# Kernel optimization log

Measured on AMD Instinct MI355X. Metric: run time of the kernel, lower is better.

## Reference

```python
import jax, jax.numpy as jnp
import numpy as np

N = 100000      # nodes
E = 1600000     # edges (avg degree 16)
IN_DIM = 128
H = 4           # num_heads
D = 16          # out_feats per head
EF = 32         # edge_feats
T = 8           # num_etypes
NEG_SLOPE = 0.2


def setup_inputs() -> dict:
    key = jax.random.key(0)
    ks = jax.random.split(key, 10)
    x = jax.random.normal(ks[0], (N, IN_DIM), dtype=jnp.float32)
    src = jax.random.randint(ks[1], (E,), 0, N)
    dst = jax.random.randint(ks[2], (E,), 0, N)
    etype = jax.random.randint(ks[3], (E,), 0, T)
    # learned params (xavier-ish scale)
    fc_W = jax.random.normal(ks[4], (IN_DIM, H * D), dtype=jnp.float32) * (2.0 / (IN_DIM + H * D)) ** 0.5
    fc_e_W = jax.random.normal(ks[5], (EF, H * EF), dtype=jnp.float32) * (2.0 / (EF + H * EF)) ** 0.5
    edge_emb = jax.random.normal(ks[6], (T, EF), dtype=jnp.float32)
    attn_l = jax.random.normal(ks[7], (H, D), dtype=jnp.float32) * (2.0 / (H * D)) ** 0.5
    attn_r = jax.random.normal(ks[8], (H, D), dtype=jnp.float32) * (2.0 / (H * D)) ** 0.5
    attn_e = jax.random.normal(ks[9], (H, EF), dtype=jnp.float32) * (2.0 / (H * EF)) ** 0.5
    return {"x": x, "src": src, "dst": dst, "etype": etype,
            "fc_W": fc_W, "fc_e_W": fc_e_W, "edge_emb": edge_emb,
            "attn_l": attn_l, "attn_r": attn_r, "attn_e": attn_e}


def reference(x, src, dst, etype, fc_W, fc_e_W, edge_emb, attn_l, attn_r, attn_e):
    n = x.shape[0]
    # node projection: [N, H, D]
    feat = (x @ fc_W).reshape(n, H, D)
    el = jnp.einsum('nhd,hd->nh', feat, attn_l)   # [N, H]
    er = jnp.einsum('nhd,hd->nh', feat, attn_r)   # [N, H]
    # per-etype edge scalar: edge_emb @ fc_e -> [T, H, EF] -> [T, H]
    ef = (edge_emb @ fc_e_W).reshape(T, H, EF)
    ee = jnp.einsum('the,he->th', ef, attn_e)
    # per-edge attention logits, leaky relu  [E, H]
    s = jax.nn.leaky_relu(el[src] + er[dst] + ee[etype], NEG_SLOPE)
    # edge_softmax over incoming edges of each dst (homogeneous graph)
    smax = jax.ops.segment_max(s, dst, num_segments=n)
    p = jnp.exp(s - smax[dst])
    denom = jax.ops.segment_sum(p, dst, num_segments=n)
    a = p / denom[dst]                             # [E, H]
    # gather-mul-scatter aggregation: sum_e a_e * feat[src_e]
    msg = feat[src] * a[:, :, None]                # [E, H, D]
    rst = jax.ops.segment_sum(msg, dst, num_segments=n)  # [N, H, D]
    return rst
```

## Files before the change

kernel.cpp:

```cpp
#include <hip/hip_runtime.h>

#define NH 4
#define HD 64
#define IN_DIM 128
#define NEG_SLOPE 0.2f
#define BN 256
#define NBMAX 512
#define SLAB 5120
#define CHUNK 4096
#define EPT (CHUNK/512)
#define SBUFSZ SLAB
#define NGEMM 391

typedef short bf8 __attribute__((ext_vector_type(8)));
typedef float f4  __attribute__((ext_vector_type(4)));

__device__ inline unsigned short f2bf(float f) {
  unsigned u = __float_as_uint(f);
  u += 0x7FFFu + ((u >> 16) & 1u);
  return (unsigned short)(u >> 16);
}

__global__ __launch_bounds__(512) void k_combo(
    const float* __restrict__ x, const float* __restrict__ fcW,
    const float* __restrict__ attn_l, const float* __restrict__ attn_r,
    unsigned short* __restrict__ featb, float4* __restrict__ el4, float4* __restrict__ er4,
    const int* __restrict__ src, const int* __restrict__ dst, const int* __restrict__ et,
    int* __restrict__ cntg, unsigned* __restrict__ ebuf,
    const float* __restrict__ edge_emb, const float* __restrict__ fc_e_W,
    const float* __restrict__ attn_e, float* __restrict__ ee,
    int n, int ne, int nb, int ngemm, int nchunks)
{
  __shared__ union {
    struct {
      int scnt[NBMAX];
      unsigned short sbase[NBMAX];
      unsigned short goff[NBMAX];
      unsigned sbuf[CHUNK];
      int wsm[8], wbs[8];
    } m;
    unsigned short wt[HD][IN_DIM + 8];
    float sef[8][128];
  } sm;

  const int t = threadIdx.x;
  const int lane = t & 63, wv = t >> 6;

  if (blockIdx.x < ngemm) {
    for (int idx = t; idx < IN_DIM * HD; idx += 512) {
      int k = idx >> 6, j = idx & 63;
      sm.wt[j][k] = f2bf(fcW[idx]);
    }
    __syncthreads();

    const int lr = lane & 15;
    const int lg = lane >> 4;
    float al[NH], ar[NH];
#pragma unroll
    for (int h = 0; h < NH; ++h) { al[h] = attn_l[h * 16 + lr]; ar[h] = attn_r[h * 16 + lr]; }

    const int ntp = (n + 127) >> 7;
    for (int tp = blockIdx.x; tp < ntp; tp += ngemm) {
      const int rowbase = tp * 128 + wv * 16;
      int arow = rowbase + lr;
      if (arow >= n) arow = n - 1;
      const float* xp = x + (size_t)arow * IN_DIM + lg * 8;

      f4 acc[4] = {};
#pragma unroll
      for (int kc = 0; kc < 4; ++kc) {
        float4 a0 = *(const float4*)(xp + kc * 32);
        float4 a1 = *(const float4*)(xp + kc * 32 + 4);
        bf8 af;
        af[0] = (short)f2bf(a0.x); af[1] = (short)f2bf(a0.y);
        af[2] = (short)f2bf(a0.z); af[3] = (short)f2bf(a0.w);
        af[4] = (short)f2bf(a1.x); af[5] = (short)f2bf(a1.y);
        af[6] = (short)f2bf(a1.z); af[7] = (short)f2bf(a1.w);
#pragma unroll
        for (int nt = 0; nt < 4; ++nt) {
          bf8 bfr = *(const bf8*)&sm.wt[nt * 16 + lr][kc * 32 + lg * 8];
          acc[nt] = __builtin_amdgcn_mfma_f32_16x16x32_bf16(af, bfr, acc[nt], 0, 0, 0);
        }
      }

#pragma unroll
      for (int r = 0; r < 4; ++r) {
        int grow = rowbase + lg * 4 + r;
        bool ok = grow < n;
        if (ok) {
#pragma unroll
          for (int nt = 0; nt < 4; ++nt)
            featb[(size_t)grow * HD + nt * 16 + lr] = f2bf(acc[nt][r]);
        }
        float pl[NH], pr[NH];
#pragma unroll
        for (int h = 0; h < NH; ++h) { pl[h] = acc[h][r] * al[h]; pr[h] = acc[h][r] * ar[h]; }
#pragma unroll
        for (int off = 1; off < 16; off <<= 1) {
#pragma unroll
          for (int h = 0; h < NH; ++h) {
            pl[h] += __shfl_xor(pl[h], off);
            pr[h] += __shfl_xor(pr[h], off);
          }
        }
        if (ok && lr == 0) {
          el4[grow] = make_float4(pl[0], pl[1], pl[2], pl[3]);
          er4[grow] = make_float4(pr[0], pr[1], pr[2], pr[3]);
        }
      }
    }
    return;
  }

  if (blockIdx.x >= ngemm + nchunks) {
    if (t < 128) {
      for (int r = 0; r < 8; ++r) {
        float acc = 0.f;
#pragma unroll
        for (int k = 0; k < 32; ++k) acc = fmaf(edge_emb[r * 32 + k], fc_e_W[k * 128 + t], acc);
        sm.sef[r][t] = acc;
      }
    }
    __syncthreads();
    if (t < 32) {
      int r = t >> 2, h = t & 3;
      float acc = 0.f;
#pragma unroll
      for (int e2 = 0; e2 < 32; ++e2) acc += sm.sef[r][h * 32 + e2] * attn_e[h * 32 + e2];
      ee[r * NH + h] = acc;
    }
    return;
  }

  const int base = (blockIdx.x - ngemm) * CHUNK;
  for (int i = t; i < nb; i += 512) sm.m.scnt[i] = 0;
  __syncthreads();
  unsigned pk[EPT], rc[EPT];
#pragma unroll
  for (int i = 0; i < EPT; ++i) {
    int e = base + i * 512 + t;
    pk[i] = 0xFFFFFFFFu;
    if (e < ne) {
      int d = dst[e];
      int bin = d >> 8;
      rc[i] = (unsigned)src[e] | ((unsigned)et[e] << 17) | ((unsigned)(d & 255) << 20);
      int slot = atomicAdd(&sm.m.scnt[bin], 1);
      pk[i] = ((unsigned)slot << 9) | (unsigned)bin;
    }
  }
  __syncthreads();
  int c = (t < nb) ? sm.m.scnt[t] : 0;
  int inc = c;
#pragma unroll
  for (int off = 1; off < 64; off <<= 1) {
    int v = __shfl_up(inc, off);
    if (lane >= off) inc += v;
  }
  if (lane == 63) sm.m.wsm[wv] = inc;
  __syncthreads();
  if (t == 0) { int r = 0; for (int k = 0; k < 8; ++k) { sm.m.wbs[k] = r; r += sm.m.wsm[k]; } }
  __syncthreads();
  int ex = sm.m.wbs[wv] + inc - c;
  if (t < nb) {
    sm.m.sbase[t] = (unsigned short)ex;
    if (c > 0) {
      int raw = atomicAdd(&cntg[t], c);
      sm.m.goff[t] = (unsigned short)(raw < SLAB ? raw : SLAB);
    }
  }
  __syncthreads();
#pragma unroll
  for (int i = 0; i < EPT; ++i) {
    if (pk[i] != 0xFFFFFFFFu) {
      int bin = (int)(pk[i] & 511u);
      int slot = (int)(pk[i] >> 9);
      sm.m.sbuf[(int)sm.m.sbase[bin] + slot] = rc[i];
    }
  }
  __syncthreads();
  const int sub = lane >> 3, rl = lane & 7;
  for (int b0 = wv * 8 + sub; b0 < nb; b0 += 64) {
    int cnt = sm.m.scnt[b0];
    if (cnt > 0) {
      int sb = (int)sm.m.sbase[b0];
      int go = (int)sm.m.goff[b0];
      int allowed = SLAB - go;
      if (allowed > cnt) allowed = cnt;
      unsigned* gp = ebuf + (size_t)b0 * SLAB + go;
      for (int i2 = rl; i2 < allowed; i2 += 8)
        gp[i2] = sm.m.sbuf[sb + i2];
    }
  }
}

__global__ __launch_bounds__(1024) void k_sortagg(
    const unsigned* __restrict__ ebuf, const int* __restrict__ cntg,
    const float* __restrict__ el, const float4* __restrict__ er4,
    const float* __restrict__ eeg, const uint4* __restrict__ featq,
    const int* __restrict__ src, const int* __restrict__ dst, const int* __restrict__ et,
    float4* __restrict__ out4, int n, int ne)
{
  __shared__ unsigned sbuf[SBUFSZ];
  __shared__ int cnt[BN];
  __shared__ int sb[BN + 1];
  __shared__ float s_er[BN][NH];
  __shared__ float s_ee[32];
  __shared__ int wsum[4];
  const int t = threadIdx.x;
  const int node0 = blockIdx.x * BN;
  const int count0 = cntg[blockIdx.x];
  const int count = count0 < SLAB ? count0 : SLAB;
  const int beg = blockIdx.x * SLAB;
  const int end = beg + count;
  for (int i = t; i < BN; i += 1024) {
    cnt[i] = 0;
    int node = node0 + i;
    float4 v = (node < n) ? er4[node] : make_float4(0.f, 0.f, 0.f, 0.f);
    s_er[i][0] = v.x; s_er[i][1] = v.y; s_er[i][2] = v.z; s_er[i][3] = v.w;
  }
  if (t < 32) s_ee[t] = eeg[t];
  __syncthreads();

  const int lane = t & 63, wv = t >> 6;
  const int q = lane >> 3;
  const int l = lane & 7;
  const int h = l >> 1;
  const bool sorted = (count0 <= SLAB);

  if (sorted) {
    unsigned rr_[(SBUFSZ + 1023) / 1024], pk_[(SBUFSZ + 1023) / 1024];
#pragma unroll
    for (int j = 0; j < (SBUFSZ + 1023) / 1024; ++j) {
      int i = beg + j * 1024 + t;
      pk_[j] = 0xFFFFFFFFu;
      if (i < end) {
        unsigned r = ebuf[i];
        rr_[j] = r;
        unsigned bin = r >> 20;
        unsigned slot = (unsigned)atomicAdd(&cnt[bin], 1);
        pk_[j] = (slot << 8) | bin;
      }
    }
    __syncthreads();
    int cc = 0, inc = 0;
    if (t < BN) {
      cc = cnt[t];
      inc = cc;
#pragma unroll
      for (int off = 1; off < 64; off <<= 1) {
        int v = __shfl_up(inc, off);
        if (lane >= off) inc += v;
      }
      if (lane == 63) wsum[wv] = inc;
    }
    __syncthreads();
    if (t < BN) {
      int base = 0;
#pragma unroll
      for (int k = 0; k < 4; ++k) if (k < wv) base += wsum[k];
      int ex = base + inc - cc;
      sb[t] = ex;
      if (t == BN - 1) sb[BN] = ex + cc;
    }
    __syncthreads();
#pragma unroll
    for (int j = 0; j < (SBUFSZ + 1023) / 1024; ++j) {
      if (pk_[j] != 0xFFFFFFFFu)
        sbuf[sb[pk_[j] & 255u] + (int)(pk_[j] >> 8)] = rr_[j];
    }
    __syncthreads();
  }

  for (int ld = wv * 16; ld < wv * 16 + 16; ++ld) {
    float erh = s_er[ld][h];
    float a0 = 0.f, a1 = 0.f, a2 = 0.f, a3 = 0.f;
    float a4 = 0.f, a5 = 0.f, a6 = 0.f, a7 = 0.f, den = 0.f;
    if (sorted) {
      const int s0 = sb[ld], s1 = sb[ld + 1];
      for (int i = s0 + q; i < s1; i += 8) {
        unsigned r = sbuf[i];
        int s  = (int)(r & 0x1FFFFu);
        int tt = (int)((r >> 17) & 7u);
        float sv = el[s * NH + h] + erh + s_ee[tt * NH + h];
        sv = sv > 0.f ? sv : NEG_SLOPE * sv;
        float p = __expf(sv);
        den += p;
        uint4 u = featq[(size_t)s * 8 + l];
        a0 = fmaf(p, __uint_as_float(u.x << 16), a0);
        a1 = fmaf(p, __uint_as_float(u.x & 0xFFFF0000u), a1);
        a2 = fmaf(p, __uint_as_float(u.y << 16), a2);
        a3 = fmaf(p, __uint_as_float(u.y & 0xFFFF0000u), a3);
        a4 = fmaf(p, __uint_as_float(u.z << 16), a4);
        a5 = fmaf(p, __uint_as_float(u.z & 0xFFFF0000u), a5);
        a6 = fmaf(p, __uint_as_float(u.w << 16), a6);
        a7 = fmaf(p, __uint_as_float(u.w & 0xFFFF0000u), a7);
      }
    } else {
      int node = node0 + ld;
      for (int i = q; i < ne; i += 8) {
        if (dst[i] != node) continue;
        int s  = src[i];
        int tt = et[i];
        float sv = el[s * NH + h] + erh + s_ee[tt * NH + h];
        sv = sv > 0.f ? sv : NEG_SLOPE * sv;
        float p = __expf(sv);
        den += p;
        uint4 u = featq[(size_t)s * 8 + l];
        a0 = fmaf(p, __uint_as_float(u.x << 16), a0);
        a1 = fmaf(p, __uint_as_float(u.x & 0xFFFF0000u), a1);
        a2 = fmaf(p, __uint_as_float(u.y << 16), a2);
        a3 = fmaf(p, __uint_as_float(u.y & 0xFFFF0000u), a3);
        a4 = fmaf(p, __uint_as_float(u.z << 16), a4);
        a5 = fmaf(p, __uint_as_float(u.z & 0xFFFF0000u), a5);
        a6 = fmaf(p, __uint_as_float(u.w << 16), a6);
        a7 = fmaf(p, __uint_as_float(u.w & 0xFFFF0000u), a7);
      }
    }
#pragma unroll
    for (int off = 8; off <= 32; off <<= 1) {
      den += __shfl_xor(den, off);
      a0 += __shfl_xor(a0, off); a1 += __shfl_xor(a1, off);
      a2 += __shfl_xor(a2, off); a3 += __shfl_xor(a3, off);
      a4 += __shfl_xor(a4, off); a5 += __shfl_xor(a5, off);
      a6 += __shfl_xor(a6, off); a7 += __shfl_xor(a7, off);
    }
    if (q == 0) {
      int node = node0 + ld;
      if (node < n) {
        float inv = den > 0.f ? 1.f / den : 0.f;
        float4* op = out4 + (size_t)node * 16 + l * 2;
        op[0] = make_float4(a0 * inv, a1 * inv, a2 * inv, a3 * inv);
        op[1] = make_float4(a4 * inv, a5 * inv, a6 * inv, a7 * inv);
      }
    }
  }
}

extern "C" void kernel_launch(void* const* d_in, const int* in_sizes, int n_in,
                              void* d_out, int out_size, void* d_ws, size_t ws_size,
                              hipStream_t stream)
{
  const float* x        = (const float*)d_in[0];
  const int*   src      = (const int*)d_in[1];
  const int*   dst      = (const int*)d_in[2];
  const int*   etype    = (const int*)d_in[3];
  const float* fcW      = (const float*)d_in[4];
  const float* fceW     = (const float*)d_in[5];
  const float* edge_emb = (const float*)d_in[6];
  const float* attn_l   = (const float*)d_in[7];
  const float* attn_r   = (const float*)d_in[8];
  const float* attn_e   = (const float*)d_in[9];
  float* out = (float*)d_out;

  const int n  = in_sizes[0] / IN_DIM;
  const int ne = in_sizes[1];
  const int nb = (n + BN - 1) / BN;
  const int nchunks = (ne + CHUNK - 1) / CHUNK;

  char* ws = (char*)d_ws;
  size_t off = 0;
  unsigned short* featb = (unsigned short*)(ws + off); off += (size_t)n * HD * sizeof(unsigned short);
  float* el    = (float*)(ws + off); off += (size_t)n * NH * sizeof(float);
  float* er    = (float*)(ws + off); off += (size_t)n * NH * sizeof(float);
  float* ee    = (float*)(ws + off); off += 256;
  int* cntg    = (int*)(ws + off);   off += NBMAX * sizeof(int);
  unsigned* ebuf = (unsigned*)(ws + off); off += (size_t)NBMAX * SLAB * sizeof(unsigned);

  hipMemsetAsync(cntg, 0, NBMAX * sizeof(int), stream);

  k_combo<<<NGEMM + nchunks + 1, 512, 0, stream>>>(
      x, fcW, attn_l, attn_r, featb, (float4*)el, (float4*)er,
      src, dst, etype, cntg, ebuf, edge_emb, fceW, attn_e, ee,
      n, ne, nb, NGEMM, nchunks);
  k_sortagg<<<nb, 1024, 0, stream>>>(ebuf, cntg, el, (const float4*)er, ee,
                                     (const uint4*)featb, src, dst, etype,
                                     (float4*)out, n, ne);
}
```

Measured before the change: 104.8 us.

## Split each node bucket across two half-size blocks in sort-aggregate kernel

Launches two 512-thread blocks per 256-node bucket instead of one 1024-thread block. Each block filters the bucket's edge slab for its 128-node half, then sorts and aggregates only those edges. This increases grid parallelism and reduces shared memory per block, which may improve occupancy and load balance. In exchange, each edge slab is read twice from global memory, and a new overflow check falls back to the unsorted path when a half exceeds the smaller buffer.

```diff
diff --git a/kernel.cpp b/kernel.cpp
--- a/kernel.cpp
+++ b/kernel.cpp
@@ -9,7 +9,7 @@
 #define SLAB 5120
 #define CHUNK 4096
 #define EPT (CHUNK/512)
-#define SBUFSZ SLAB
+#define HSBUF 4096
 #define NGEMM 391
 
 typedef short bf8 __attribute__((ext_vector_type(8)));
@@ -193,80 +193,87 @@
   }
 }
 
-__global__ __launch_bounds__(1024) void k_sortagg(
+__global__ __launch_bounds__(512) void k_sortagg(
     const unsigned* __restrict__ ebuf, const int* __restrict__ cntg,
     const float* __restrict__ el, const float4* __restrict__ er4,
     const float* __restrict__ eeg, const uint4* __restrict__ featq,
     const int* __restrict__ src, const int* __restrict__ dst, const int* __restrict__ et,
     float4* __restrict__ out4, int n, int ne)
 {
-  __shared__ unsigned sbuf[SBUFSZ];
-  __shared__ int cnt[BN];
-  __shared__ int sb[BN + 1];
-  __shared__ float s_er[BN][NH];
+  __shared__ unsigned sbuf[HSBUF];
+  __shared__ int cnt[128];
+  __shared__ int sb[129];
+  __shared__ float s_er[128][NH];
   __shared__ float s_ee[32];
-  __shared__ int wsum[4];
+  __shared__ int wsum[2];
+  __shared__ int ovf;
   const int t = threadIdx.x;
-  const int node0 = blockIdx.x * BN;
-  const int count0 = cntg[blockIdx.x];
+  const int bb = blockIdx.x >> 1;
+  const int hh = blockIdx.x & 1;
+  const int node0 = bb * BN + hh * 128;
+  const int count0 = cntg[bb];
   const int count = count0 < SLAB ? count0 : SLAB;
-  const int beg = blockIdx.x * SLAB;
+  const int beg = bb * SLAB;
   const int end = beg + count;
-  for (int i = t; i < BN; i += 1024) {
-    cnt[i] = 0;
-    int node = node0 + i;
-    float4 v = (node < n) ? er4[node] : make_float4(0.f, 0.f, 0.f, 0.f);
-    s_er[i][0] = v.x; s_er[i][1] = v.y; s_er[i][2] = v.z; s_er[i][3] = v.w;
+  for (int i = t; i < 128; i += 512) cnt[i] = 0;
+  {
+    int i = t & 127;
+    if (t < 128) {
+      int node = node0 + i;
+      float4 v = (node < n) ? er4[node] : make_float4(0.f, 0.f, 0.f, 0.f);
+      s_er[i][0] = v.x; s_er[i][1] = v.y; s_er[i][2] = v.z; s_er[i][3] = v.w;
+    }
   }
   if (t < 32) s_ee[t] = eeg[t];
+  if (t == 0) ovf = (count0 > SLAB) ? 1 : 0;
   __syncthreads();
 
   const int lane = t & 63, wv = t >> 6;
   const int q = lane >> 3;
   const int l = lane & 7;
   const int h = l >> 1;
-  const bool sorted = (count0 <= SLAB);
-
+
+  unsigned rr_[SLAB / 512], pk_[SLAB / 512];
+#pragma unroll
+  for (int j = 0; j < SLAB / 512; ++j) {
+    int i = beg + j * 512 + t;
+    pk_[j] = 0xFFFFFFFFu;
+    if (i < end) {
+      unsigned r = ebuf[i];
+      unsigned dl = r >> 20;
+      if ((int)(dl >> 7) == hh) {
+        rr_[j] = r;
+        unsigned bin = dl & 127u;
+        unsigned slot = (unsigned)atomicAdd(&cnt[bin], 1);
+        pk_[j] = (slot << 7) | bin;
+      }
+    }
+  }
+  __syncthreads();
+  int cc = 0, inc = 0;
+  if (t < 128) {
+    cc = cnt[t];
+    inc = cc;
+#pragma unroll
+    for (int off = 1; off < 64; off <<= 1) {
+      int v = __shfl_up(inc, off);
+      if (lane >= off) inc += v;
+    }
+    if (lane == 63) wsum[wv] = inc;
+  }
+  __syncthreads();
+  if (t < 128) {
+    int ex = (wv ? wsum[0] : 0) + inc - cc;
+    sb[t] = ex;
+    if (t == 127) { sb[128] = ex + cc; if (ex + cc > HSBUF) atomicOr(&ovf, 1); }
+  }
+  __syncthreads();
+  const bool sorted = (ovf == 0);
   if (sorted) {
-    unsigned rr_[(SBUFSZ + 1023) / 1024], pk_[(SBUFSZ + 1023) / 1024];
-#pragma unroll
-    for (int j = 0; j < (SBUFSZ + 1023) / 1024; ++j) {
-      int i = beg + j * 1024 + t;
-      pk_[j] = 0xFFFFFFFFu;
-      if (i < end) {
-        unsigned r = ebuf[i];
-        rr_[j] = r;
-        unsigned bin = r >> 20;
-        unsigned slot = (unsigned)atomicAdd(&cnt[bin], 1);
-        pk_[j] = (slot << 8) | bin;
-      }
-    }
-    __syncthreads();
-    int cc = 0, inc = 0;
-    if (t < BN) {
-      cc = cnt[t];
-      inc = cc;
-#pragma unroll
-      for (int off = 1; off < 64; off <<= 1) {
-        int v = __shfl_up(inc, off);
-        if (lane >= off) inc += v;
-      }
-      if (lane == 63) wsum[wv] = inc;
-    }
-    __syncthreads();
-    if (t < BN) {
-      int base = 0;
-#pragma unroll
-      for (int k = 0; k < 4; ++k) if (k < wv) base += wsum[k];
-      int ex = base + inc - cc;
-      sb[t] = ex;
-      if (t == BN - 1) sb[BN] = ex + cc;
-    }
-    __syncthreads();
-#pragma unroll
-    for (int j = 0; j < (SBUFSZ + 1023) / 1024; ++j) {
+#pragma unroll
+    for (int j = 0; j < SLAB / 512; ++j) {
       if (pk_[j] != 0xFFFFFFFFu)
-        sbuf[sb[pk_[j] & 255u] + (int)(pk_[j] >> 8)] = rr_[j];
+        sbuf[sb[pk_[j] & 127u] + (int)(pk_[j] >> 7)] = rr_[j];
     }
     __syncthreads();
   }
@@ -372,7 +379,7 @@
       x, fcW, attn_l, attn_r, featb, (float4*)el, (float4*)er,
       src, dst, etype, cntg, ebuf, edge_emb, fceW, attn_e, ee,
       n, ne, nb, NGEMM, nchunks);
-  k_sortagg<<<nb, 1024, 0, stream>>>(ebuf, cntg, el, (const float4*)er, ee,
-                                     (const uint4*)featb, src, dst, etype,
-                                     (float4*)out, n, ne);
+  k_sortagg<<<2 * nb, 512, 0, stream>>>(ebuf, cntg, el, (const float4*)er, ee,
+                                        (const uint4*)featb, src, dst, etype,
+                                        (float4*)out, n, ne);
 }
```

New measurement: 105.2 us. About the same (+0.4%).
